# Kernel optimization log

Hardware: AMD Instinct MI355X
Metric: run time of the kernel (lower is better)

## Reference

```python
import jax, jax.numpy as jnp
import numpy as np

# Problem dims (see shape_source)
M_MACH = 50          # n_machines
N_JOBS = 100         # n_jobs
MT_BITS = 4          # machine_time_bits (capped at 4)
JS_BITS = 2          # job_status_bits (capped at 2)
OBS = M_MACH + N_JOBS + M_MACH * N_JOBS          # 5150
F = M_MACH * MT_BITS + N_JOBS * JS_BITS + M_MACH * N_JOBS  # 5400 total binary features
A = 32               # number of actions (one Tsetlin machine each)
C = 1000             # clauses per TM (min(nr_of_clauses, 1000))
INIT = 16            # TA-state include/exclude threshold


def setup_inputs() -> dict:
    key = jax.random.key(0)
    k1, k2, k3, k4, k5 = jax.random.split(key, 5)
    # state = [machine_times | job_status | op_status]; op_status is binary in the env
    machine_times = jax.random.uniform(k1, (M_MACH,), dtype=jnp.float32) * 100.0
    job_status = jax.random.uniform(k2, (N_JOBS,), dtype=jnp.float32)
    op_status = jax.random.randint(k3, (M_MACH * N_JOBS,), 0, 2).astype(jnp.float32)
    state = jnp.concatenate([machine_times, job_status, op_status])
    # TA states in [1, 32); >16 means literal is included. int8 as in the torch module.
    ta_state = jax.random.randint(k4, (A, C, 2, F), 1, 32).astype(jnp.int8)
    # clause signs in {+1, -1}
    clause_sign = (2 * jax.random.randint(k5, (A, C), 0, 2) - 1).astype(jnp.int8)
    return {"state": state, "ta_state": ta_state, "clause_sign": clause_sign}


def _binary_encode(state):
    """JSSPFeatureTransformer.transform: state -> [F] int32 binary features."""
    mt = state[:M_MACH]
    mx = jnp.max(mt)
    safe_mx = jnp.where(mx > 0, mx, jnp.float32(1.0))
    # if max_time == 0 the torch code leaves these bits at zero; where() matches that
    norm = jnp.where(mx > 0, mt / safe_mx * (2 ** MT_BITS - 1), 0.0).astype(jnp.int32)
    mt_bits = ((norm[:, None] // (2 ** jnp.arange(MT_BITS, dtype=jnp.int32))) % 2).reshape(-1)
    js = state[M_MACH:M_MACH + N_JOBS]
    status = jnp.minimum((js * (2 ** JS_BITS - 1)).astype(jnp.int32), 2 ** JS_BITS - 1)
    js_bits = ((status[:, None] // (2 ** jnp.arange(JS_BITS, dtype=jnp.int32))) % 2).reshape(-1)
    op_bits = state[M_MACH + N_JOBS:].astype(jnp.int32)
    return jnp.concatenate([mt_bits, js_bits, op_bits])  # [F]


def reference(state, ta_state, clause_sign):
    feats = _binary_encode(state)                         # [F] int32 in {0,1}
    ta = ta_state.astype(jnp.int8)
    include = ta[:, :, 0, :] > INIT                       # [A,C,F]
    exclude = ta[:, :, 1, :] > INIT                       # [A,C,F]
    f0 = (feats == 0)[None, None, :]
    f1 = (feats == 1)[None, None, :]
    violations = jnp.any((include & f0) | (exclude & f1), axis=-1)  # [A,C]
    clause_out = (~violations).astype(jnp.int32)          # [A,C]
    # pos_sum - neg_sum == sum(clause_out * sign) with sign in {+1,-1}
    q_values = jnp.sum(clause_out * clause_sign.astype(jnp.int32), axis=-1)
    return q_values.astype(jnp.float32)                   # [A]
```

## Files before the change

### kernel.cpp

```cpp
#include <hip/hip_runtime.h>
#include <stdint.h>

#define M_MACH 50
#define N_JOBS 100
#define NFEAT 5400
#define A_DIM 32
#define C_DIM 1000
#define INIT_T 16
#define WAVES_PER_BLOCK 8

__global__ __launch_bounds__(512) void fused_clause_kernel(
    const float* __restrict__ state,
    const int8_t* __restrict__ ta,
    const int8_t* __restrict__ sign,
    float* __restrict__ out) {
    const int lane = threadIdx.x & 63;
    const int wid  = threadIdx.x >> 6;
    const int q    = blockIdx.x * WAVES_PER_BLOCK + wid;
    const int8_t* base = ta + (size_t)q * (2 * NFEAT);

    const int in0 = base[lane];
    const int ex0 = base[NFEAT + lane];

    const float v0 = (lane < M_MACH) ? state[lane] : -1.0f;
    float mx = v0;
    #pragma unroll
    for (int off = 1; off < 64; off <<= 1)
        mx = fmaxf(mx, __shfl_xor(mx, off, 64));

    const float s_i = __shfl(v0, lane >> 2, 64);
    const int norm = (mx > 0.0f) ? (int)((s_i / mx) * 15.0f) : 0;
    const int bit  = (norm >> (lane & 3)) & 1;

    const bool v = ((bit ? ex0 : in0) > INIT_T);
    if (__any(v)) return;

    for (int f0 = 64; f0 < NFEAT; f0 += 64) {
        const int f = f0 + lane;
        bool vv = false;
        if (f < NFEAT) {
            int b;
            if (f < M_MACH * 4) {
                const int i = f >> 2;
                const int n2 = (mx > 0.0f) ? (int)((state[i] / mx) * 15.0f) : 0;
                b = (n2 >> (f & 3)) & 1;
            } else if (f < M_MACH * 4 + N_JOBS * 2) {
                const int rel = f - M_MACH * 4;
                const int j = rel >> 1;
                int st = (int)(state[M_MACH + j] * 3.0f);
                if (st > 3) st = 3;
                b = (st >> (rel & 1)) & 1;
            } else {
                b = (int)state[M_MACH + N_JOBS + (f - (M_MACH*4 + N_JOBS*2))];
            }
            vv = ((b ? base[NFEAT + f] : base[f]) > INIT_T);
        }
        if (__any(vv)) return;
    }

    if (lane == 0) atomicAdd(&out[q / C_DIM], (float)sign[q]);
}

extern "C" void kernel_launch(void* const* d_in, const int* in_sizes, int n_in,
                              void* d_out, int out_size, void* d_ws, size_t ws_size,
                              hipStream_t stream) {
    const float*  state = (const float*)d_in[0];
    const int8_t* ta    = (const int8_t*)d_in[1];
    const int8_t* sign  = (const int8_t*)d_in[2];
    float* out = (float*)d_out;

    hipMemsetAsync(out, 0, out_size * sizeof(float), stream);

    fused_clause_kernel<<<4000, 512, 0, stream>>>(state, ta, sign, out);
}
```

Baseline: 13.89 us.

## Assign one block per action with persistent waves and block-level reduction

Replaces the 4000-block grid (one wave per clause, atomics into the output) with 32 blocks, one per action, where 16 waves loop over clauses with a one-ahead prefetch of the first 64 TA bytes. Partial sums are reduced in shared memory and written directly, which removes the memset and the atomics. The cost is much lower parallelism: only 32 CUs are used, and each wave processes about 63 clauses serially, so load latency is exposed on every clause.

After: 18.54 us. +33.4%, slower.

```diff
diff --git a/kernel.cpp b/kernel.cpp
--- a/kernel.cpp
+++ b/kernel.cpp
@@ -7,58 +7,83 @@
 #define A_DIM 32
 #define C_DIM 1000
 #define INIT_T 16
-#define WAVES_PER_BLOCK 8
+#define WPB 16
 
-__global__ __launch_bounds__(512) void fused_clause_kernel(
+__global__ __launch_bounds__(1024) void policy_kernel(
     const float* __restrict__ state,
     const int8_t* __restrict__ ta,
     const int8_t* __restrict__ sign,
     float* __restrict__ out) {
     const int lane = threadIdx.x & 63;
     const int wid  = threadIdx.x >> 6;
-    const int q    = blockIdx.x * WAVES_PER_BLOCK + wid;
-    const int8_t* base = ta + (size_t)q * (2 * NFEAT);
-
-    const int in0 = base[lane];
-    const int ex0 = base[NFEAT + lane];
+    const int a    = blockIdx.x;
 
     const float v0 = (lane < M_MACH) ? state[lane] : -1.0f;
     float mx = v0;
     #pragma unroll
     for (int off = 1; off < 64; off <<= 1)
         mx = fmaxf(mx, __shfl_xor(mx, off, 64));
+    const float s_i = __shfl(v0, lane >> 2, 64);
+    const int norm  = (mx > 0.0f) ? (int)((s_i / mx) * 15.0f) : 0;
+    const bool bit  = (norm >> (lane & 3)) & 1;
 
-    const float s_i = __shfl(v0, lane >> 2, 64);
-    const int norm = (mx > 0.0f) ? (int)((s_i / mx) * 15.0f) : 0;
-    const int bit  = (norm >> (lane & 3)) & 1;
+    int psum = 0;
+    int c = wid;
+    int8_t cin = 0, cex = 0;
+    if (c < C_DIM) {
+        const int8_t* b = ta + ((size_t)a * C_DIM + c) * (2 * NFEAT);
+        cin = b[lane];
+        cex = b[NFEAT + lane];
+    }
+    while (c < C_DIM) {
+        const int cn = c + WPB;
+        int8_t nin = 0, nex = 0;
+        if (cn < C_DIM) {
+            const int8_t* b = ta + ((size_t)a * C_DIM + cn) * (2 * NFEAT);
+            nin = b[lane];
+            nex = b[NFEAT + lane];
+        }
 
-    const bool v = ((bit ? ex0 : in0) > INIT_T);
-    if (__any(v)) return;
+        bool violated = __any((bit ? cex : cin) > INIT_T);
+        if (!violated) {
+            const int q = a * C_DIM + c;
+            const int8_t* base = ta + (size_t)q * (2 * NFEAT);
+            for (int f0 = 64; f0 < NFEAT && !violated; f0 += 64) {
+                const int f = f0 + lane;
+                bool vv = false;
+                if (f < NFEAT) {
+                    int b2;
+                    if (f < M_MACH * 4) {
+                        const int i = f >> 2;
+                        const int n2 = (mx > 0.0f) ? (int)((state[i] / mx) * 15.0f) : 0;
+                        b2 = (n2 >> (f & 3)) & 1;
+                    } else if (f < M_MACH * 4 + N_JOBS * 2) {
+                        const int rel = f - M_MACH * 4;
+                        int st = (int)(state[M_MACH + (rel >> 1)] * 3.0f);
+                        if (st > 3) st = 3;
+                        b2 = (st >> (rel & 1)) & 1;
+                    } else {
+                        b2 = (int)state[M_MACH + N_JOBS + (f - (M_MACH*4 + N_JOBS*2))];
+                    }
+                    vv = ((b2 ? base[NFEAT + f] : base[f]) > INIT_T);
+                }
+                violated = __any(vv);
+            }
+            if (!violated) psum += (int)sign[q];
+        }
 
-    for (int f0 = 64; f0 < NFEAT; f0 += 64) {
-        const int f = f0 + lane;
-        bool vv = false;
-        if (f < NFEAT) {
-            int b;
-            if (f < M_MACH * 4) {
-                const int i = f >> 2;
-                const int n2 = (mx > 0.0f) ? (int)((state[i] / mx) * 15.0f) : 0;
-                b = (n2 >> (f & 3)) & 1;
-            } else if (f < M_MACH * 4 + N_JOBS * 2) {
-                const int rel = f - M_MACH * 4;
-                const int j = rel >> 1;
-                int st = (int)(state[M_MACH + j] * 3.0f);
-                if (st > 3) st = 3;
-                b = (st >> (rel & 1)) & 1;
-            } else {
-                b = (int)state[M_MACH + N_JOBS + (f - (M_MACH*4 + N_JOBS*2))];
-            }
-            vv = ((b ? base[NFEAT + f] : base[f]) > INIT_T);
-        }
-        if (__any(vv)) return;
+        cin = nin; cex = nex; c = cn;
     }
 
-    if (lane == 0) atomicAdd(&out[q / C_DIM], (float)sign[q]);
+    __shared__ int red[WPB];
+    if (lane == 0) red[wid] = psum;
+    __syncthreads();
+    if (threadIdx.x == 0) {
+        int t = 0;
+        #pragma unroll
+        for (int i = 0; i < WPB; ++i) t += red[i];
+        out[a] = (float)t;
+    }
 }
 
 extern "C" void kernel_launch(void* const* d_in, const int* in_sizes, int n_in,
@@ -69,7 +94,5 @@
     const int8_t* sign  = (const int8_t*)d_in[2];
     float* out = (float*)d_out;
 
-    hipMemsetAsync(out, 0, out_size * sizeof(float), stream);
-
-    fused_clause_kernel<<<4000, 512, 0, stream>>>(state, ta, sign, out);
+    policy_kernel<<<A_DIM, WPB * 64, 0, stream>>>(state, ta, sign, out);
 }
```

## Map one clause per thread and test first 16 features with packed-byte compares

Applied to the files above, without the earlier changes.

Each clause is now handled by a single thread instead of a whole wave. The launch drops from 4000 blocks of 512 threads to 125 blocks of 256. Each thread loads 16 include and 16 exclude bytes as 64-bit words, builds a byte mask from the machine-time bits via a ballot, and checks all 16 literals at once with SWAR byte arithmetic. Only if no violation is found there does it fall back to a serial per-feature loop. This removes most of the wave scheduling and cross-lane reduction cost, in exchange for uncoalesced strided loads and a slow serial path for clauses that survive the first 16 features.

Measured after the change: 26.01 us. 87.2% more time.

```diff
diff --git a/kernel.cpp b/kernel.cpp
--- a/kernel.cpp
+++ b/kernel.cpp
@@ -7,20 +7,21 @@
 #define A_DIM 32
 #define C_DIM 1000
 #define INIT_T 16
-#define WAVES_PER_BLOCK 8
 
-__global__ __launch_bounds__(512) void fused_clause_kernel(
+__global__ __launch_bounds__(256) void policy_kernel(
     const float* __restrict__ state,
     const int8_t* __restrict__ ta,
     const int8_t* __restrict__ sign,
     float* __restrict__ out) {
     const int lane = threadIdx.x & 63;
     const int wid  = threadIdx.x >> 6;
-    const int q    = blockIdx.x * WAVES_PER_BLOCK + wid;
+    const int q    = (blockIdx.x * 4 + wid) * 64 + lane;
+
     const int8_t* base = ta + (size_t)q * (2 * NFEAT);
-
-    const int in0 = base[lane];
-    const int ex0 = base[NFEAT + lane];
+    const uint64_t in01 = *reinterpret_cast<const uint64_t*>(base);
+    const uint64_t in23 = *reinterpret_cast<const uint64_t*>(base + 8);
+    const uint64_t ex01 = *reinterpret_cast<const uint64_t*>(base + NFEAT);
+    const uint64_t ex23 = *reinterpret_cast<const uint64_t*>(base + NFEAT + 8);
 
     const float v0 = (lane < M_MACH) ? state[lane] : -1.0f;
     float mx = v0;
@@ -28,37 +29,56 @@
     for (int off = 1; off < 64; off <<= 1)
         mx = fmaxf(mx, __shfl_xor(mx, off, 64));
 
-    const float s_i = __shfl(v0, lane >> 2, 64);
-    const int norm = (mx > 0.0f) ? (int)((s_i / mx) * 15.0f) : 0;
-    const int bit  = (norm >> (lane & 3)) & 1;
+    bool mybit = false;
+    if (lane < 16) {
+        const float s = __shfl(v0, lane >> 2, 64);
+        const int n = (mx > 0.0f) ? (int)((s / mx) * 15.0f) : 0;
+        mybit = (n >> (lane & 3)) & 1;
+    }
+    const uint32_t mask16 = (uint32_t)(__ballot(mybit) & 0xFFFFull);
 
-    const bool v = ((bit ? ex0 : in0) > INIT_T);
-    if (__any(v)) return;
+    uint32_t M[4];
+    #pragma unroll
+    for (int d = 0; d < 4; ++d) {
+        const uint32_t nib = (mask16 >> (4 * d)) & 0xFu;
+        M[d] = ((nib * 0x00204081u) & 0x01010101u) * 0xFFu;
+    }
 
-    for (int f0 = 64; f0 < NFEAT; f0 += 64) {
-        const int f = f0 + lane;
-        bool vv = false;
-        if (f < NFEAT) {
+    const uint32_t in_d[4] = { (uint32_t)in01, (uint32_t)(in01 >> 32),
+                               (uint32_t)in23, (uint32_t)(in23 >> 32) };
+    const uint32_t ex_d[4] = { (uint32_t)ex01, (uint32_t)(ex01 >> 32),
+                               (uint32_t)ex23, (uint32_t)(ex23 >> 32) };
+
+    uint32_t acc = 0;
+    #pragma unroll
+    for (int d = 0; d < 4; ++d) {
+        const uint32_t sel = (in_d[d] & ~M[d]) | (ex_d[d] & M[d]);
+        acc |= ((sel & 0x7F7F7F7Fu) + 0x6F6F6F6Fu) | sel;
+    }
+    bool violated = (acc & 0x80808080u) != 0u;
+
+    int val = 0;
+    if (!violated) {
+        bool bad = false;
+        for (int f = 16; f < NFEAT && !bad; ++f) {
             int b;
             if (f < M_MACH * 4) {
-                const int i = f >> 2;
-                const int n2 = (mx > 0.0f) ? (int)((state[i] / mx) * 15.0f) : 0;
-                b = (n2 >> (f & 3)) & 1;
+                const int n = (mx > 0.0f)
+                    ? (int)((state[f >> 2] / mx) * 15.0f) : 0;
+                b = (n >> (f & 3)) & 1;
             } else if (f < M_MACH * 4 + N_JOBS * 2) {
                 const int rel = f - M_MACH * 4;
-                const int j = rel >> 1;
-                int st = (int)(state[M_MACH + j] * 3.0f);
+                int st = (int)(state[M_MACH + (rel >> 1)] * 3.0f);
                 if (st > 3) st = 3;
                 b = (st >> (rel & 1)) & 1;
             } else {
                 b = (int)state[M_MACH + N_JOBS + (f - (M_MACH*4 + N_JOBS*2))];
             }
-            vv = ((b ? base[NFEAT + f] : base[f]) > INIT_T);
+            bad = ((b ? base[NFEAT + f] : base[f]) > INIT_T);
         }
-        if (__any(vv)) return;
+        if (!bad) val = (int)sign[q];
     }
-
-    if (lane == 0) atomicAdd(&out[q / C_DIM], (float)sign[q]);
+    if (val != 0) atomicAdd(&out[q / C_DIM], (float)val);
 }
 
 extern "C" void kernel_launch(void* const* d_in, const int* in_sizes, int n_in,
@@ -71,5 +91,5 @@
 
     hipMemsetAsync(out, 0, out_size * sizeof(float), stream);
 
-    fused_clause_kernel<<<4000, 512, 0, stream>>>(state, ta, sign, out);
+    policy_kernel<<<125, 256, 0, stream>>>(state, ta, sign, out);
 }
```

## Pack two clauses per wavefront with half-wave first-chunk early exit

Applied to the files above, without the earlier changes.

Each 64-lane wavefront now checks the first 32 features of two clauses at once, one per half-wave, and combines the results with a single ballot. Only clauses that survive that first chunk go on to a full-wave scan of the remaining features. The grid is halved to 2000 blocks. Since random TA states make almost every clause fail within the first few features, this aims to halve the wave count and launch/scheduling overhead, at the cost of a narrower first probe and a serialized fallback loop.

Measured after the change: 13.73 us. Within noise of the previous version (-1.2%).

```diff
diff --git a/kernel.cpp b/kernel.cpp
--- a/kernel.cpp
+++ b/kernel.cpp
@@ -7,20 +7,23 @@
 #define A_DIM 32
 #define C_DIM 1000
 #define INIT_T 16
-#define WAVES_PER_BLOCK 8
+#define WPB 8
 
-__global__ __launch_bounds__(512) void fused_clause_kernel(
+__global__ __launch_bounds__(512) void policy_kernel(
     const float* __restrict__ state,
     const int8_t* __restrict__ ta,
     const int8_t* __restrict__ sign,
     float* __restrict__ out) {
     const int lane = threadIdx.x & 63;
     const int wid  = threadIdx.x >> 6;
-    const int q    = blockIdx.x * WAVES_PER_BLOCK + wid;
+    const int sub  = lane & 31;
+    const int half = lane >> 5;
+    const int q0   = (blockIdx.x * WPB + wid) * 2;
+    const int q    = q0 + half;
+
     const int8_t* base = ta + (size_t)q * (2 * NFEAT);
-
-    const int in0 = base[lane];
-    const int ex0 = base[NFEAT + lane];
+    const int inb = base[sub];
+    const int exb = base[NFEAT + sub];
 
     const float v0 = (lane < M_MACH) ? state[lane] : -1.0f;
     float mx = v0;
@@ -28,37 +31,47 @@
     for (int off = 1; off < 64; off <<= 1)
         mx = fmaxf(mx, __shfl_xor(mx, off, 64));
 
-    const float s_i = __shfl(v0, lane >> 2, 64);
-    const int norm = (mx > 0.0f) ? (int)((s_i / mx) * 15.0f) : 0;
-    const int bit  = (norm >> (lane & 3)) & 1;
+    const float s_i = __shfl(v0, sub >> 2, 64);
+    const int norm  = (mx > 0.0f) ? (int)((s_i / mx) * 15.0f) : 0;
+    const bool bit  = (norm >> (sub & 3)) & 1;
 
-    const bool v = ((bit ? ex0 : in0) > INIT_T);
-    if (__any(v)) return;
+    const unsigned long long ball = __ballot((bit ? exb : inb) > INIT_T);
+    const bool violated = half ? (ball >> 32) != 0ull
+                               : (ball & 0xFFFFFFFFull) != 0ull;
 
-    for (int f0 = 64; f0 < NFEAT; f0 += 64) {
-        const int f = f0 + lane;
-        bool vv = false;
-        if (f < NFEAT) {
-            int b;
-            if (f < M_MACH * 4) {
-                const int i = f >> 2;
-                const int n2 = (mx > 0.0f) ? (int)((state[i] / mx) * 15.0f) : 0;
-                b = (n2 >> (f & 3)) & 1;
-            } else if (f < M_MACH * 4 + N_JOBS * 2) {
-                const int rel = f - M_MACH * 4;
-                const int j = rel >> 1;
-                int st = (int)(state[M_MACH + j] * 3.0f);
-                if (st > 3) st = 3;
-                b = (st >> (rel & 1)) & 1;
-            } else {
-                b = (int)state[M_MACH + N_JOBS + (f - (M_MACH*4 + N_JOBS*2))];
+    bool ok = !violated;
+    #pragma unroll 1
+    for (int j = 0; j < 2; ++j) {
+        const bool need = __shfl(ok ? 1 : 0, j * 32, 64);
+        if (!need) continue;
+        const int qq = q0 + j;
+        const int8_t* b0 = ta + (size_t)qq * (2 * NFEAT);
+        bool viol = false;
+        for (int f0 = 32; f0 < NFEAT && !viol; f0 += 64) {
+            const int f = f0 + lane;
+            bool vv = false;
+            if (f < NFEAT) {
+                int b2;
+                if (f < M_MACH * 4) {
+                    const int n2 = (mx > 0.0f)
+                        ? (int)((state[f >> 2] / mx) * 15.0f) : 0;
+                    b2 = (n2 >> (f & 3)) & 1;
+                } else if (f < M_MACH * 4 + N_JOBS * 2) {
+                    const int rel = f - M_MACH * 4;
+                    int st = (int)(state[M_MACH + (rel >> 1)] * 3.0f);
+                    if (st > 3) st = 3;
+                    b2 = (st >> (rel & 1)) & 1;
+                } else {
+                    b2 = (int)state[M_MACH + N_JOBS + (f - (M_MACH*4 + N_JOBS*2))];
+                }
+                vv = ((b2 ? b0[NFEAT + f] : b0[f]) > INIT_T);
             }
-            vv = ((b ? base[NFEAT + f] : base[f]) > INIT_T);
+            viol = __any(vv);
         }
-        if (__any(vv)) return;
+        if (viol && half == j) ok = false;
     }
 
-    if (lane == 0) atomicAdd(&out[q / C_DIM], (float)sign[q]);
+    if (ok && sub == 0) atomicAdd(&out[q / C_DIM], (float)sign[q]);
 }
 
 extern "C" void kernel_launch(void* const* d_in, const int* in_sizes, int n_in,
@@ -71,5 +84,5 @@
 
     hipMemsetAsync(out, 0, out_size * sizeof(float), stream);
 
-    fused_clause_kernel<<<4000, 512, 0, stream>>>(state, ta, sign, out);
+    policy_kernel<<<2000, 512, 0, stream>>>(state, ta, sign, out);
 }
```
